# Kernel optimization log

Measured on AMD Instinct MI355X. Metric: run time of the kernel, lower is better.

## Reference

```python
import jax, jax.numpy as jnp
import numpy as np

N_NODES = 100000

def setup_inputs() -> dict:
    key = jax.random.key(0)
    ks = jax.random.split(key, 6)
    x = jax.random.normal(ks[0], (N_NODES, 128), dtype=jnp.float32)
    edge_index = jax.random.randint(ks[1], (2, 600000), 0, N_NODES, dtype=jnp.int64)
    W_self = jax.random.normal(ks[2], (128, 128), dtype=jnp.float32) * 0.05
    b_self = jax.random.normal(ks[3], (128,), dtype=jnp.float32) * 0.05
    W_neigh = jax.random.normal(ks[4], (128, 128), dtype=jnp.float32) * 0.05
    b_neigh = jax.random.normal(ks[5], (128,), dtype=jnp.float32) * 0.05
    return {"x": x, "edge_index": edge_index, "W_self": W_self, "b_self": b_self,
            "W_neigh": W_neigh, "b_neigh": b_neigh}

def reference(x, edge_index, W_self, b_self, W_neigh, b_neigh):
    src, dst = edge_index[0], edge_index[1]
    n = x.shape[0]
    # scatter-add of gathered neighbor features: agg[dst] += x[src]
    agg = jax.ops.segment_sum(x[src], dst, num_segments=n)            # [N, d]
    deg = jax.ops.segment_sum(jnp.ones_like(dst, dtype=x.dtype), dst,
                              num_segments=n)                         # [N]
    agg = agg / jnp.clip(deg, 1.0, None)[:, None]                     # mean aggregation
    h = x @ W_self.T + b_self + agg @ W_neigh.T + b_neigh
    return jax.nn.relu(h)  # dropout=0.0 -> identity
```

## Files before the change

### kernel.cpp

```cpp
#include <hip/hip_runtime.h>

#define N_NODES 100000
#define N_EDGES 600000
#define D 128
#define RPB 32
#define NBLK (N_NODES / RPB)
#define CAPN 31
#define AK 264
#define GSCALE (7.0f / 127.0f)
#define GINV   (127.0f / 7.0f)

typedef __attribute__((ext_vector_type(8))) short short8;
typedef __attribute__((ext_vector_type(4))) float f32x4;

static __device__ __forceinline__ short f2bf(float f) {
    union { float f; unsigned u; } v; v.f = f;
    unsigned r = v.u + 0x7fffu + ((v.u >> 16) & 1u);
    return (short)(r >> 16);
}
static __device__ __forceinline__ float bf2f(short s) {
    union { unsigned u; float f; } c; c.u = ((unsigned)(unsigned short)s) << 16; return c.f;
}
static __device__ __forceinline__ int q8(float v) {
    int b = (int)rintf(v * GINV);
    return b < -127 ? -127 : (b > 127 ? 127 : b);
}

__global__ __launch_bounds__(256) void init_nd_g8(const float* __restrict__ x,
                                                  const float* __restrict__ Ws,
                                                  const float* __restrict__ Wn,
                                                  const int* __restrict__ src,
                                                  const int* __restrict__ dst,
                                                  short* __restrict__ x_bf,
                                                  unsigned char* __restrict__ x_i8,
                                                  short* __restrict__ Wcat,
                                                  int* __restrict__ nd) {
    int t = blockIdx.x * 256 + threadIdx.x;
    if (t < N_NODES * 16) {
        const float4* xp = reinterpret_cast<const float4*>(x + (size_t)t * 8);
        float4 v0 = xp[0], v1 = xp[1];
        short8 p;
        p[0] = f2bf(v0.x); p[1] = f2bf(v0.y); p[2] = f2bf(v0.z); p[3] = f2bf(v0.w);
        p[4] = f2bf(v1.x); p[5] = f2bf(v1.y); p[6] = f2bf(v1.z); p[7] = f2bf(v1.w);
        *reinterpret_cast<short8*>(x_bf + (size_t)t * 8) = p;

        int b0 = q8(v0.x), b1 = q8(v0.y), b2 = q8(v0.z), b3 = q8(v0.w);
        int b4 = q8(v1.x), b5 = q8(v1.y), b6 = q8(v1.z), b7 = q8(v1.w);
        unsigned lo = (unsigned)(b0 & 0xff) | ((unsigned)(b1 & 0xff) << 8)
                    | ((unsigned)(b2 & 0xff) << 16) | ((unsigned)(b3 & 0xff) << 24);
        unsigned hi = (unsigned)(b4 & 0xff) | ((unsigned)(b5 & 0xff) << 8)
                    | ((unsigned)(b6 & 0xff) << 16) | ((unsigned)(b7 & 0xff) << 24);
        *reinterpret_cast<uint2*>(x_i8 + (size_t)t * 8) = make_uint2(lo, hi);
    }
    if (t < N_EDGES) {
        int d = dst[t];
        int* line = nd + (size_t)d * 32;
        int pos = atomicAdd(line, 1);
        if (pos < CAPN) line[1 + pos] = src[t];
    }
    if (t < 2 * D * D) {
        int n = t >> 8, k = t & 255;
        float v = (k < D) ? Ws[n * D + k] : Wn[n * D + (k - D)];
        Wcat[t] = f2bf(v);
    }
}

__global__ __launch_bounds__(512, 4) void fused_sage_v9(const short* __restrict__ x_bf,
                                                        const unsigned char* __restrict__ x_i8,
                                                        const int* __restrict__ nd,
                                                        const short* __restrict__ Wcat,
                                                        const float* __restrict__ bs,
                                                        const float* __restrict__ bn,
                                                        float* __restrict__ out) {
    __shared__ short As[RPB][AK];

    int tid = threadIdx.x;
    int row0 = blockIdx.x * RPB;

    {
        int r = tid >> 4;
        int c = (tid & 15) * 8;
        *reinterpret_cast<short8*>(&As[r][c]) =
            *reinterpret_cast<const short8*>(x_bf + (size_t)(row0 + r) * D + c);
    }

    {
        int g = tid >> 4;
        int l = tid & 15;
        int v = row0 + g;
        const int* line = nd + (size_t)v * 32;
        int dv = line[0];
        int n = dv < CAPN ? dv : CAPN;
        const int* sl = line + 1;
        short8 pk;
        #pragma unroll
        for (int k = 0; k < 8; ++k) pk[k] = 0;
        if (n > 0) {
            int acc[8] = {};
            int id[8]; bool okm[8];
            #pragma unroll
            for (int j = 0; j < 8; ++j) {
                okm[j] = j < n;
                id[j] = okm[j] ? sl[j] : v;
            }
            #pragma unroll
            for (int j = 0; j < 8; ++j) {
                uint2 q = *reinterpret_cast<const uint2*>(x_i8 + (size_t)id[j] * D + l * 8);
                unsigned qx = okm[j] ? q.x : 0u;
                unsigned qy = okm[j] ? q.y : 0u;
                acc[0] += (int)(signed char)(qx);
                acc[1] += (int)(signed char)(qx >> 8);
                acc[2] += (int)(signed char)(qx >> 16);
                acc[3] += (int)(signed char)(qx >> 24);
                acc[4] += (int)(signed char)(qy);
                acc[5] += (int)(signed char)(qy >> 8);
                acc[6] += (int)(signed char)(qy >> 16);
                acc[7] += (int)(signed char)(qy >> 24);
            }
            for (int e = 8; e < n; e += 4) {
                int id2[4]; bool ok2[4];
                #pragma unroll
                for (int j = 0; j < 4; ++j) {
                    ok2[j] = (e + j) < n;
                    id2[j] = ok2[j] ? sl[e + j] : v;
                }
                #pragma unroll
                for (int j = 0; j < 4; ++j) {
                    uint2 q = *reinterpret_cast<const uint2*>(x_i8 + (size_t)id2[j] * D + l * 8);
                    unsigned qx = ok2[j] ? q.x : 0u;
                    unsigned qy = ok2[j] ? q.y : 0u;
                    acc[0] += (int)(signed char)(qx);
                    acc[1] += (int)(signed char)(qx >> 8);
                    acc[2] += (int)(signed char)(qx >> 16);
                    acc[3] += (int)(signed char)(qx >> 24);
                    acc[4] += (int)(signed char)(qy);
                    acc[5] += (int)(signed char)(qy >> 8);
                    acc[6] += (int)(signed char)(qy >> 16);
                    acc[7] += (int)(signed char)(qy >> 24);
                }
            }
            float dq = GSCALE / fmaxf((float)dv, 1.0f);
            #pragma unroll
            for (int k = 0; k < 8; ++k) pk[k] = f2bf((float)acc[k] * dq);
        }
        *reinterpret_cast<short8*>(&As[g][D + l * 8]) = pk;
    }
    __syncthreads();

    {
        int wv = tid >> 6;
        int l  = tid & 63;
        int lr = l & 15;
        int lk = (l >> 4) * 8;
        int n0 = wv * 16;

        f32x4 acc0 = {}, acc1 = {};
        #pragma unroll
        for (int kb = 0; kb < 8; ++kb) {
            short8 a0 = *reinterpret_cast<const short8*>(&As[lr][kb * 32 + lk]);
            short8 a1 = *reinterpret_cast<const short8*>(&As[16 + lr][kb * 32 + lk]);
            short8 bb = *reinterpret_cast<const short8*>(
                Wcat + (size_t)(n0 + lr) * 256 + kb * 32 + lk);
            acc0 = __builtin_amdgcn_mfma_f32_16x16x32_bf16(a0, bb, acc0, 0, 0, 0);
            acc1 = __builtin_amdgcn_mfma_f32_16x16x32_bf16(a1, bb, acc1, 0, 0, 0);
        }

        int lq = (l >> 4) * 4;
        int col = n0 + lr;
        float bias = bs[col] + bn[col];
        #pragma unroll
        for (int j = 0; j < 4; ++j)
            out[(size_t)(row0 + lq + j) * D + col] = fmaxf(acc0[j] + bias, 0.0f);
        #pragma unroll
        for (int j = 0; j < 4; ++j)
            out[(size_t)(row0 + 16 + lq + j) * D + col] = fmaxf(acc1[j] + bias, 0.0f);
    }
}

__global__ __launch_bounds__(256) void init_slots(const float* __restrict__ x,
                                                  const float* __restrict__ Ws,
                                                  const float* __restrict__ Wn,
                                                  const int* __restrict__ src,
                                                  const int* __restrict__ dst,
                                                  short* __restrict__ x_bf,
                                                  short* __restrict__ Wcat,
                                                  int* __restrict__ deg,
                                                  int* __restrict__ slots) {
    int t = blockIdx.x * 256 + threadIdx.x;
    if (t < (N_NODES * D) / 8) {
        const float4* xp = reinterpret_cast<const float4*>(x + (size_t)t * 8);
        float4 v0 = xp[0], v1 = xp[1];
        short8 p;
        p[0] = f2bf(v0.x); p[1] = f2bf(v0.y); p[2] = f2bf(v0.z); p[3] = f2bf(v0.w);
        p[4] = f2bf(v1.x); p[5] = f2bf(v1.y); p[6] = f2bf(v1.z); p[7] = f2bf(v1.w);
        *reinterpret_cast<short8*>(x_bf + (size_t)t * 8) = p;
    }
    if (t < N_EDGES) {
        int d = dst[t];
        int pos = atomicAdd(&deg[d], 1);
        if (pos < 28) slots[(size_t)d * 28 + pos] = src[t];
    }
    if (t < 2 * D * D) {
        int n = t >> 8, k = t & 255;
        float v = (k < D) ? Ws[n * D + k] : Wn[n * D + (k - D)];
        Wcat[t] = f2bf(v);
    }
}

__global__ __launch_bounds__(512, 4) void fused_sage_v5(const short* __restrict__ x_bf,
                                                        const int* __restrict__ deg,
                                                        const int* __restrict__ slots,
                                                        const short* __restrict__ Wcat,
                                                        const float* __restrict__ bs,
                                                        const float* __restrict__ bn,
                                                        float* __restrict__ out) {
    __shared__ short As[RPB][AK];
    int tid = threadIdx.x;
    int row0 = blockIdx.x * RPB;
    {
        int r = tid >> 4;
        int c = (tid & 15) * 8;
        *reinterpret_cast<short8*>(&As[r][c]) =
            *reinterpret_cast<const short8*>(x_bf + (size_t)(row0 + r) * D + c);
    }
    {
        int g = tid >> 4;
        int l = tid & 15;
        int v = row0 + g;
        int dv = deg[v];
        int n = dv < 28 ? dv : 28;
        const int* sl = slots + (size_t)v * 28;
        short8 pk;
        #pragma unroll
        for (int k = 0; k < 8; ++k) pk[k] = 0;
        if (n > 0) {
            float acc[8] = {};
            int id[8]; float wt[8];
            #pragma unroll
            for (int j = 0; j < 8; ++j) {
                bool ok = j < n;
                id[j] = ok ? sl[j] : v;
                wt[j] = ok ? 1.0f : 0.0f;
            }
            #pragma unroll
            for (int j = 0; j < 8; ++j) {
                short8 a = *reinterpret_cast<const short8*>(x_bf + (size_t)id[j] * D + l * 8);
                #pragma unroll
                for (int k = 0; k < 8; ++k) acc[k] += wt[j] * bf2f(a[k]);
            }
            for (int e = 8; e < n; e += 4) {
                int id2[4]; float wt2[4];
                #pragma unroll
                for (int j = 0; j < 4; ++j) {
                    bool ok = (e + j) < n;
                    id2[j] = ok ? sl[e + j] : v;
                    wt2[j] = ok ? 1.0f : 0.0f;
                }
                #pragma unroll
                for (int j = 0; j < 4; ++j) {
                    short8 a = *reinterpret_cast<const short8*>(x_bf + (size_t)id2[j] * D + l * 8);
                    #pragma unroll
                    for (int k = 0; k < 8; ++k) acc[k] += wt2[j] * bf2f(a[k]);
                }
            }
            float inv = 1.0f / fmaxf((float)dv, 1.0f);
            #pragma unroll
            for (int k = 0; k < 8; ++k) pk[k] = f2bf(acc[k] * inv);
        }
        *reinterpret_cast<short8*>(&As[g][D + l * 8]) = pk;
    }
    __syncthreads();
    {
        int wv = tid >> 6;
        int l  = tid & 63;
        int lr = l & 15;
        int lk = (l >> 4) * 8;
        int n0 = wv * 16;
        f32x4 acc0 = {}, acc1 = {};
        #pragma unroll
        for (int kb = 0; kb < 8; ++kb) {
            short8 a0 = *reinterpret_cast<const short8*>(&As[lr][kb * 32 + lk]);
            short8 a1 = *reinterpret_cast<const short8*>(&As[16 + lr][kb * 32 + lk]);
            short8 bb = *reinterpret_cast<const short8*>(
                Wcat + (size_t)(n0 + lr) * 256 + kb * 32 + lk);
            acc0 = __builtin_amdgcn_mfma_f32_16x16x32_bf16(a0, bb, acc0, 0, 0, 0);
            acc1 = __builtin_amdgcn_mfma_f32_16x16x32_bf16(a1, bb, acc1, 0, 0, 0);
        }
        int lq = (l >> 4) * 4;
        int col = n0 + lr;
        float bias = bs[col] + bn[col];
        #pragma unroll
        for (int j = 0; j < 4; ++j)
            out[(size_t)(row0 + lq + j) * D + col] = fmaxf(acc0[j] + bias, 0.0f);
        #pragma unroll
        for (int j = 0; j < 4; ++j)
            out[(size_t)(row0 + 16 + lq + j) * D + col] = fmaxf(acc1[j] + bias, 0.0f);
    }
}

extern "C" void kernel_launch(void* const* d_in, const int* in_sizes, int n_in,
                              void* d_out, int out_size, void* d_ws, size_t ws_size,
                              hipStream_t stream) {
    const float* x  = (const float*)d_in[0];
    const int*   ei = (const int*)d_in[1];
    const float* Ws = (const float*)d_in[2];
    const float* bs = (const float*)d_in[3];
    const float* Wn = (const float*)d_in[4];
    const float* bn = (const float*)d_in[5];
    float* out = (float*)d_out;

    const int* src = ei;
    const int* dst = ei + N_EDGES;

    size_t need_nd = (size_t)N_NODES * 32 * 4 + (size_t)2 * D * D * 2
                   + (size_t)N_NODES * D * 2 + (size_t)N_NODES * D;

    if (ws_size >= need_nd) {
        int* nd     = (int*)d_ws;
        short* Wcat = (short*)(nd + (size_t)N_NODES * 32);
        short* x_bf = Wcat + 2 * D * D;
        unsigned char* x_i8 = (unsigned char*)(x_bf + (size_t)N_NODES * D);

        hipMemsetAsync(nd, 0, (size_t)N_NODES * 32 * sizeof(int), stream);
        init_nd_g8<<<(N_NODES * 16 + 255) / 256, 256, 0, stream>>>(
            x, Ws, Wn, src, dst, x_bf, x_i8, Wcat, nd);
        fused_sage_v9<<<NBLK, 512, 0, stream>>>(x_bf, x_i8, nd, Wcat, bs, bn, out);
    } else {
        int* deg    = (int*)d_ws;
        int* slots  = deg + N_NODES;
        short* Wcat = (short*)(slots + (size_t)N_NODES * 28);
        short* x_bf = Wcat + 2 * D * D;

        hipMemsetAsync(deg, 0, N_NODES * sizeof(int), stream);
        init_slots<<<(N_NODES * 16 + 255) / 256, 256, 0, stream>>>(
            x, Ws, Wn, src, dst, x_bf, Wcat, deg, slots);
        fused_sage_v5<<<NBLK, 512, 0, stream>>>(x_bf, deg, slots, Wcat, bs, bn, out);
    }
}
```

Measured before the change: 100.4 us.

## Fuse memset, preprocessing and SAGE compute into one cooperative persistent kernel

The separate memset, the init kernel and the fused aggregation/GEMM kernel are replaced by a single cooperative kernel of 512 blocks × 512 threads. It zeroes the neighbor lists, converts x and the weights, scatters the edges, and runs the gather+MFMA stage, with grid-wide syncs between phases. This removes the launch gaps between kernels. In exchange it adds two grid barriers and a persistent loop over 3125 row tiles on 512 blocks, which leaves the last pass uneven. The fallback branch now uses the same large workspace layout as the main path, even though it runs only when the workspace is smaller.

```diff
diff --git a/kernel.cpp b/kernel.cpp
--- a/kernel.cpp
+++ b/kernel.cpp
@@ -1,4 +1,7 @@
 #include <hip/hip_runtime.h>
+#include <hip/hip_cooperative_groups.h>
+
+namespace cg = cooperative_groups;
 
 #define N_NODES 100000
 #define N_EDGES 600000
@@ -9,6 +12,8 @@
 #define AK 264
 #define GSCALE (7.0f / 127.0f)
 #define GINV   (127.0f / 7.0f)
+#define CBLKS 512
+#define CTHR  512
 
 typedef __attribute__((ext_vector_type(8))) short short8;
 typedef __attribute__((ext_vector_type(4))) float f32x4;
@@ -24,6 +29,165 @@
 static __device__ __forceinline__ int q8(float v) {
     int b = (int)rintf(v * GINV);
     return b < -127 ? -127 : (b > 127 ? 127 : b);
+}
+
+__global__ __launch_bounds__(CTHR, 4) void sage_coop(const float* __restrict__ x,
+                                                     const float* __restrict__ Ws,
+                                                     const float* __restrict__ Wn,
+                                                     const int* __restrict__ src,
+                                                     const int* __restrict__ dst,
+                                                     short* __restrict__ x_bf,
+                                                     unsigned char* __restrict__ x_i8,
+                                                     short* __restrict__ Wcat,
+                                                     int* __restrict__ nd,
+                                                     const float* __restrict__ bs,
+                                                     const float* __restrict__ bn,
+                                                     float* __restrict__ out) {
+    cg::grid_group grid = cg::this_grid();
+    __shared__ short As[RPB][AK];
+
+    const int tid = threadIdx.x;
+    const int gtid = blockIdx.x * CTHR + tid;
+    const int nthr = CBLKS * CTHR;
+
+    {
+        uint4 z = make_uint4(0, 0, 0, 0);
+        for (int i = gtid; i < N_NODES * 8; i += nthr)
+            reinterpret_cast<uint4*>(nd)[i] = z;
+        for (int t = gtid; t < N_NODES * 16; t += nthr) {
+            const float4* xp = reinterpret_cast<const float4*>(x + (size_t)t * 8);
+            float4 v0 = xp[0], v1 = xp[1];
+            short8 p;
+            p[0] = f2bf(v0.x); p[1] = f2bf(v0.y); p[2] = f2bf(v0.z); p[3] = f2bf(v0.w);
+            p[4] = f2bf(v1.x); p[5] = f2bf(v1.y); p[6] = f2bf(v1.z); p[7] = f2bf(v1.w);
+            *reinterpret_cast<short8*>(x_bf + (size_t)t * 8) = p;
+            int b0 = q8(v0.x), b1 = q8(v0.y), b2 = q8(v0.z), b3 = q8(v0.w);
+            int b4 = q8(v1.x), b5 = q8(v1.y), b6 = q8(v1.z), b7 = q8(v1.w);
+            unsigned lo = (unsigned)(b0 & 0xff) | ((unsigned)(b1 & 0xff) << 8)
+                        | ((unsigned)(b2 & 0xff) << 16) | ((unsigned)(b3 & 0xff) << 24);
+            unsigned hi = (unsigned)(b4 & 0xff) | ((unsigned)(b5 & 0xff) << 8)
+                        | ((unsigned)(b6 & 0xff) << 16) | ((unsigned)(b7 & 0xff) << 24);
+            *reinterpret_cast<uint2*>(x_i8 + (size_t)t * 8) = make_uint2(lo, hi);
+        }
+        for (int t = gtid; t < 2 * D * D; t += nthr) {
+            int n = t >> 8, k = t & 255;
+            float v = (k < D) ? Ws[n * D + k] : Wn[n * D + (k - D)];
+            Wcat[t] = f2bf(v);
+        }
+    }
+    grid.sync();
+
+    for (int e = gtid; e < N_EDGES; e += nthr) {
+        int d = dst[e];
+        int* line = nd + (size_t)d * 32;
+        int pos = atomicAdd(line, 1);
+        if (pos < CAPN) line[1 + pos] = src[e];
+    }
+    grid.sync();
+
+    for (int b = blockIdx.x; b < NBLK; b += CBLKS) {
+        int row0 = b * RPB;
+
+        {
+            int r = tid >> 4;
+            int c = (tid & 15) * 8;
+            *reinterpret_cast<short8*>(&As[r][c]) =
+                *reinterpret_cast<const short8*>(x_bf + (size_t)(row0 + r) * D + c);
+        }
+
+        {
+            int g = tid >> 4;
+            int l = tid & 15;
+            int v = row0 + g;
+            const int* line = nd + (size_t)v * 32;
+            int dv = line[0];
+            int n = dv < CAPN ? dv : CAPN;
+            const int* sl = line + 1;
+            short8 pk;
+            #pragma unroll
+            for (int k = 0; k < 8; ++k) pk[k] = 0;
+            if (n > 0) {
+                int acc[8] = {};
+                int id[8]; bool okm[8];
+                #pragma unroll
+                for (int j = 0; j < 8; ++j) {
+                    okm[j] = j < n;
+                    id[j] = okm[j] ? sl[j] : v;
+                }
+                #pragma unroll
+                for (int j = 0; j < 8; ++j) {
+                    uint2 q = *reinterpret_cast<const uint2*>(x_i8 + (size_t)id[j] * D + l * 8);
+                    unsigned qx = okm[j] ? q.x : 0u;
+                    unsigned qy = okm[j] ? q.y : 0u;
+                    acc[0] += (int)(signed char)(qx);
+                    acc[1] += (int)(signed char)(qx >> 8);
+                    acc[2] += (int)(signed char)(qx >> 16);
+                    acc[3] += (int)(signed char)(qx >> 24);
+                    acc[4] += (int)(signed char)(qy);
+                    acc[5] += (int)(signed char)(qy >> 8);
+                    acc[6] += (int)(signed char)(qy >> 16);
+                    acc[7] += (int)(signed char)(qy >> 24);
+                }
+                for (int e = 8; e < n; e += 4) {
+                    int id2[4]; bool ok2[4];
+                    #pragma unroll
+                    for (int j = 0; j < 4; ++j) {
+                        ok2[j] = (e + j) < n;
+                        id2[j] = ok2[j] ? sl[e + j] : v;
+                    }
+                    #pragma unroll
+                    for (int j = 0; j < 4; ++j) {
+                        uint2 q = *reinterpret_cast<const uint2*>(x_i8 + (size_t)id2[j] * D + l * 8);
+                        unsigned qx = ok2[j] ? q.x : 0u;
+                        unsigned qy = ok2[j] ? q.y : 0u;
+                        acc[0] += (int)(signed char)(qx);
+                        acc[1] += (int)(signed char)(qx >> 8);
+                        acc[2] += (int)(signed char)(qx >> 16);
+                        acc[3] += (int)(signed char)(qx >> 24);
+                        acc[4] += (int)(signed char)(qy);
+                        acc[5] += (int)(signed char)(qy >> 8);
+                        acc[6] += (int)(signed char)(qy >> 16);
+                        acc[7] += (int)(signed char)(qy >> 24);
+                    }
+                }
+                float dq = GSCALE / fmaxf((float)dv, 1.0f);
+                #pragma unroll
+                for (int k = 0; k < 8; ++k) pk[k] = f2bf((float)acc[k] * dq);
+            }
+            *reinterpret_cast<short8*>(&As[g][D + l * 8]) = pk;
+        }
+        __syncthreads();
+
+        {
+            int wv = tid >> 6;
+            int l  = tid & 63;
+            int lr = l & 15;
+            int lk = (l >> 4) * 8;
+            int n0 = wv * 16;
+
+            f32x4 acc0 = {}, acc1 = {};
+            #pragma unroll
+            for (int kb = 0; kb < 8; ++kb) {
+                short8 a0 = *reinterpret_cast<const short8*>(&As[lr][kb * 32 + lk]);
+                short8 a1 = *reinterpret_cast<const short8*>(&As[16 + lr][kb * 32 + lk]);
+                short8 bb = *reinterpret_cast<const short8*>(
+                    Wcat + (size_t)(n0 + lr) * 256 + kb * 32 + lk);
+                acc0 = __builtin_amdgcn_mfma_f32_16x16x32_bf16(a0, bb, acc0, 0, 0, 0);
+                acc1 = __builtin_amdgcn_mfma_f32_16x16x32_bf16(a1, bb, acc1, 0, 0, 0);
+            }
+
+            int lq = (l >> 4) * 4;
+            int col = n0 + lr;
+            float bias = bs[col] + bn[col];
+            #pragma unroll
+            for (int j = 0; j < 4; ++j)
+                out[(size_t)(row0 + lq + j) * D + col] = fmaxf(acc0[j] + bias, 0.0f);
+            #pragma unroll
+            for (int j = 0; j < 4; ++j)
+                out[(size_t)(row0 + 16 + lq + j) * D + col] = fmaxf(acc1[j] + bias, 0.0f);
+        }
+        __syncthreads();
+    }
 }
 
 __global__ __launch_bounds__(256) void init_nd_g8(const float* __restrict__ x,
@@ -43,7 +207,6 @@
         p[0] = f2bf(v0.x); p[1] = f2bf(v0.y); p[2] = f2bf(v0.z); p[3] = f2bf(v0.w);
         p[4] = f2bf(v1.x); p[5] = f2bf(v1.y); p[6] = f2bf(v1.z); p[7] = f2bf(v1.w);
         *reinterpret_cast<short8*>(x_bf + (size_t)t * 8) = p;
-
         int b0 = q8(v0.x), b1 = q8(v0.y), b2 = q8(v0.z), b3 = q8(v0.w);
         int b4 = q8(v1.x), b5 = q8(v1.y), b6 = q8(v1.z), b7 = q8(v1.w);
         unsigned lo = (unsigned)(b0 & 0xff) | ((unsigned)(b1 & 0xff) << 8)
@@ -73,17 +236,14 @@
                                                         const float* __restrict__ bn,
                                                         float* __restrict__ out) {
     __shared__ short As[RPB][AK];
-
     int tid = threadIdx.x;
     int row0 = blockIdx.x * RPB;
-
     {
         int r = tid >> 4;
         int c = (tid & 15) * 8;
         *reinterpret_cast<short8*>(&As[r][c]) =
             *reinterpret_cast<const short8*>(x_bf + (size_t)(row0 + r) * D + c);
     }
-
     {
         int g = tid >> 4;
         int l = tid & 15;
@@ -142,130 +302,6 @@
             float dq = GSCALE / fmaxf((float)dv, 1.0f);
             #pragma unroll
             for (int k = 0; k < 8; ++k) pk[k] = f2bf((float)acc[k] * dq);
-        }
-        *reinterpret_cast<short8*>(&As[g][D + l * 8]) = pk;
-    }
-    __syncthreads();
-
-    {
-        int wv = tid >> 6;
-        int l  = tid & 63;
-        int lr = l & 15;
-        int lk = (l >> 4) * 8;
-        int n0 = wv * 16;
-
-        f32x4 acc0 = {}, acc1 = {};
-        #pragma unroll
-        for (int kb = 0; kb < 8; ++kb) {
-            short8 a0 = *reinterpret_cast<const short8*>(&As[lr][kb * 32 + lk]);
-            short8 a1 = *reinterpret_cast<const short8*>(&As[16 + lr][kb * 32 + lk]);
-            short8 bb = *reinterpret_cast<const short8*>(
-                Wcat + (size_t)(n0 + lr) * 256 + kb * 32 + lk);
-            acc0 = __builtin_amdgcn_mfma_f32_16x16x32_bf16(a0, bb, acc0, 0, 0, 0);
-            acc1 = __builtin_amdgcn_mfma_f32_16x16x32_bf16(a1, bb, acc1, 0, 0, 0);
-        }
-
-        int lq = (l >> 4) * 4;
-        int col = n0 + lr;
-        float bias = bs[col] + bn[col];
-        #pragma unroll
-        for (int j = 0; j < 4; ++j)
-            out[(size_t)(row0 + lq + j) * D + col] = fmaxf(acc0[j] + bias, 0.0f);
-        #pragma unroll
-        for (int j = 0; j < 4; ++j)
-            out[(size_t)(row0 + 16 + lq + j) * D + col] = fmaxf(acc1[j] + bias, 0.0f);
-    }
-}
-
-__global__ __launch_bounds__(256) void init_slots(const float* __restrict__ x,
-                                                  const float* __restrict__ Ws,
-                                                  const float* __restrict__ Wn,
-                                                  const int* __restrict__ src,
-                                                  const int* __restrict__ dst,
-                                                  short* __restrict__ x_bf,
-                                                  short* __restrict__ Wcat,
-                                                  int* __restrict__ deg,
-                                                  int* __restrict__ slots) {
-    int t = blockIdx.x * 256 + threadIdx.x;
-    if (t < (N_NODES * D) / 8) {
-        const float4* xp = reinterpret_cast<const float4*>(x + (size_t)t * 8);
-        float4 v0 = xp[0], v1 = xp[1];
-        short8 p;
-        p[0] = f2bf(v0.x); p[1] = f2bf(v0.y); p[2] = f2bf(v0.z); p[3] = f2bf(v0.w);
-        p[4] = f2bf(v1.x); p[5] = f2bf(v1.y); p[6] = f2bf(v1.z); p[7] = f2bf(v1.w);
-        *reinterpret_cast<short8*>(x_bf + (size_t)t * 8) = p;
-    }
-    if (t < N_EDGES) {
-        int d = dst[t];
-        int pos = atomicAdd(&deg[d], 1);
-        if (pos < 28) slots[(size_t)d * 28 + pos] = src[t];
-    }
-    if (t < 2 * D * D) {
-        int n = t >> 8, k = t & 255;
-        float v = (k < D) ? Ws[n * D + k] : Wn[n * D + (k - D)];
-        Wcat[t] = f2bf(v);
-    }
-}
-
-__global__ __launch_bounds__(512, 4) void fused_sage_v5(const short* __restrict__ x_bf,
-                                                        const int* __restrict__ deg,
-                                                        const int* __restrict__ slots,
-                                                        const short* __restrict__ Wcat,
-                                                        const float* __restrict__ bs,
-                                                        const float* __restrict__ bn,
-                                                        float* __restrict__ out) {
-    __shared__ short As[RPB][AK];
-    int tid = threadIdx.x;
-    int row0 = blockIdx.x * RPB;
-    {
-        int r = tid >> 4;
-        int c = (tid & 15) * 8;
-        *reinterpret_cast<short8*>(&As[r][c]) =
-            *reinterpret_cast<const short8*>(x_bf + (size_t)(row0 + r) * D + c);
-    }
-    {
-        int g = tid >> 4;
-        int l = tid & 15;
-        int v = row0 + g;
-        int dv = deg[v];
-        int n = dv < 28 ? dv : 28;
-        const int* sl = slots + (size_t)v * 28;
-        short8 pk;
-        #pragma unroll
-        for (int k = 0; k < 8; ++k) pk[k] = 0;
-        if (n > 0) {
-            float acc[8] = {};
-            int id[8]; float wt[8];
-            #pragma unroll
-            for (int j = 0; j < 8; ++j) {
-                bool ok = j < n;
-                id[j] = ok ? sl[j] : v;
-                wt[j] = ok ? 1.0f : 0.0f;
-            }
-            #pragma unroll
-            for (int j = 0; j < 8; ++j) {
-                short8 a = *reinterpret_cast<const short8*>(x_bf + (size_t)id[j] * D + l * 8);
-                #pragma unroll
-                for (int k = 0; k < 8; ++k) acc[k] += wt[j] * bf2f(a[k]);
-            }
-            for (int e = 8; e < n; e += 4) {
-                int id2[4]; float wt2[4];
-                #pragma unroll
-                for (int j = 0; j < 4; ++j) {
-                    bool ok = (e + j) < n;
-                    id2[j] = ok ? sl[e + j] : v;
-                    wt2[j] = ok ? 1.0f : 0.0f;
-                }
-                #pragma unroll
-                for (int j = 0; j < 4; ++j) {
-                    short8 a = *reinterpret_cast<const short8*>(x_bf + (size_t)id2[j] * D + l * 8);
-                    #pragma unroll
-                    for (int k = 0; k < 8; ++k) acc[k] += wt2[j] * bf2f(a[k]);
-                }
-            }
-            float inv = 1.0f / fmaxf((float)dv, 1.0f);
-            #pragma unroll
-            for (int k = 0; k < 8; ++k) pk[k] = f2bf(acc[k] * inv);
         }
         *reinterpret_cast<short8*>(&As[g][D + l * 8]) = pk;
     }
@@ -321,19 +357,20 @@
         short* x_bf = Wcat + 2 * D * D;
         unsigned char* x_i8 = (unsigned char*)(x_bf + (size_t)N_NODES * D);
 
+        void* args[] = { (void*)&x, (void*)&Ws, (void*)&Wn, (void*)&src, (void*)&dst,
+                         (void*)&x_bf, (void*)&x_i8, (void*)&Wcat, (void*)&nd,
+                         (void*)&bs, (void*)&bn, (void*)&out };
+        hipLaunchCooperativeKernel(reinterpret_cast<void*>(sage_coop),
+                                   dim3(CBLKS), dim3(CTHR), args, 0, stream);
+    } else {
+        int* nd     = (int*)d_ws;
+        short* Wcat = (short*)(nd + (size_t)N_NODES * 32);
+        short* x_bf = Wcat + 2 * D * D;
+        unsigned char* x_i8 = (unsigned char*)(x_bf + (size_t)N_NODES * D);
+
         hipMemsetAsync(nd, 0, (size_t)N_NODES * 32 * sizeof(int), stream);
         init_nd_g8<<<(N_NODES * 16 + 255) / 256, 256, 0, stream>>>(
             x, Ws, Wn, src, dst, x_bf, x_i8, Wcat, nd);
         fused_sage_v9<<<NBLK, 512, 0, stream>>>(x_bf, x_i8, nd, Wcat, bs, bn, out);
-    } else {
-        int* deg    = (int*)d_ws;
-        int* slots  = deg + N_NODES;
-        short* Wcat = (short*)(slots + (size_t)N_NODES * 28);
-        short* x_bf = Wcat + 2 * D * D;
-
-        hipMemsetAsync(deg, 0, N_NODES * sizeof(int), stream);
-        init_slots<<<(N_NODES * 16 + 255) / 256, 256, 0, stream>>>(
-            x, Ws, Wn, src, dst, x_bf, Wcat, deg, slots);
-        fused_sage_v5<<<NBLK, 512, 0, stream>>>(x_bf, deg, slots, Wcat, bs, bn, out);
-    }
-}
+    }
+}
```

New measurement: 235.1 us. 2.34x slower.
